# Kernel optimization log

Hardware: AMD Instinct MI355X
Metric: run time of the kernel (lower is better)

## Reference

```python
import jax, jax.numpy as jnp
import numpy as np

N_HEADS = 8
D_HEAD = 64
SCALE = D_HEAD ** -0.5


def setup_inputs() -> dict:
    key = jax.random.key(0)
    k1, k2, k3 = jax.random.split(key, 3)
    B, H, W, C = 16, 32, 32, 512
    ft = jax.random.normal(k1, (B, H, W, C), dtype=jnp.float32)
    # Dense layers: to_qkv -> n_heads*n_dim_heads*3 = 1536 units, to_out -> n_channels
    w_qkv = jax.random.normal(k2, (C, N_HEADS * D_HEAD * 3), dtype=jnp.float32) * (C ** -0.5)
    b_qkv = jnp.zeros((N_HEADS * D_HEAD * 3,), dtype=jnp.float32)
    w_out = jax.random.normal(k3, (N_HEADS * D_HEAD, C), dtype=jnp.float32) * ((N_HEADS * D_HEAD) ** -0.5)
    b_out = jnp.zeros((C,), dtype=jnp.float32)
    return {"ft": ft, "w_qkv": w_qkv, "b_qkv": b_qkv, "w_out": w_out, "b_out": b_out}


def reference(ft, w_qkv, b_qkv, w_out, b_out):
    B, H, W, C = ft.shape
    N = H * W
    x = ft.reshape(B, N, C)                       # b (h w) c
    qkv = x @ w_qkv + b_qkv                       # b n (heads * 3*d_head)
    qkv = qkv.reshape(B, N, N_HEADS, 3 * D_HEAD)  # 'b x (h d) -> b x h d'
    q, k, v = jnp.split(qkv, 3, axis=-1)          # each: b n heads d_head
    attn = jnp.einsum('bxhd,byhd->bxyh', q, k) * SCALE
    attn = jax.nn.softmax(attn, axis=2)           # softmax over key axis y
    res = jnp.einsum('bxyh,byhd->bxhd', attn, v)  # b x h d
    res = res.reshape(B, N, N_HEADS * D_HEAD)     # 'b x h d -> b x (h d)'
    res = res @ w_out + b_out
    res = res + x                                 # residual with pre-qkv flattened input
    return res.reshape(B, H, W, C)
```

## Files before the change

### kernel.cpp

```cpp
#include <hip/hip_runtime.h>
#include <hip/hip_bf16.h>

using u16 = unsigned short;
using u32 = unsigned int;
typedef __attribute__((ext_vector_type(8))) short short8;
typedef __attribute__((ext_vector_type(4))) float f32x4;

#define MFMA16(A, B, C) __builtin_amdgcn_mfma_f32_16x16x32_bf16((A), (B), (C), 0, 0, 0)

__device__ __forceinline__ u16 f2bf(float f) {
  union { float f; u32 i; } v; v.f = f;
  u32 x = v.i;
  return (u16)((x + 0x7fffu + ((x >> 16) & 1u)) >> 16);
}
__device__ __forceinline__ u32 pkbf(float a, float b) {
  union { __hip_bfloat162 h; u32 u; } v;
  v.h = __float22bfloat162_rn(make_float2(a, b));
  return v.u;
}
__device__ __forceinline__ u32 cvtpk(float a, float b) {
  u32 r;
  asm("v_cvt_pk_bf16_f32 %0, %1, %2" : "=v"(r) : "v"(a), "v"(b));
  return r;
}
__device__ __forceinline__ void gl16(const u16* g, u16* l) {
  __builtin_amdgcn_global_load_lds(
      (const __attribute__((address_space(1))) u32*)g,
      (__attribute__((address_space(3))) u32*)l, 16, 0, 0);
}

__global__ __launch_bounds__(256) void conv_x(const float* __restrict__ X,
                                              u16* __restrict__ Xbf) {
  const int i = (blockIdx.x * 256 + threadIdx.x) * 8;
  float4 a = *(const float4*)(X + i);
  float4 b = *(const float4*)(X + i + 4);
  uint4 o;
  o.x = pkbf(a.x, a.y); o.y = pkbf(a.z, a.w);
  o.z = pkbf(b.x, b.y); o.w = pkbf(b.z, b.w);
  *(uint4*)(Xbf + i) = o;
}

__global__ __launch_bounds__(256) void transpose_w(
    const float* __restrict__ Wq, const float* __restrict__ Wo,
    u16* __restrict__ Wqt, u16* __restrict__ Wot) {
  const int z = blockIdx.z;
  if (z == 1 && blockIdx.x >= 16) return;
  const float* src = z ? Wo : Wq;
  u16* dst = z ? Wot : Wqt;
  const int ncols = z ? 512 : 1536;
  __shared__ float tile[32][33];
  const int t = threadIdx.x;
  const int kt = blockIdx.y * 32, nt = blockIdx.x * 32;
  const int r = t >> 3, c4 = (t & 7) * 4;
  float4 v = *(const float4*)(src + (size_t)(kt + r) * ncols + nt + c4);
  tile[r][c4 + 0] = v.x; tile[r][c4 + 1] = v.y;
  tile[r][c4 + 2] = v.z; tile[r][c4 + 3] = v.w;
  __syncthreads();
  uint2 p = make_uint2(pkbf(tile[c4 + 0][r], tile[c4 + 1][r]),
                       pkbf(tile[c4 + 2][r], tile[c4 + 3][r]));
  *(uint2*)(dst + (size_t)(nt + r) * 512 + kt + c4) = p;
}

__global__ __launch_bounds__(512) void qkv_gemm(
    const u16* __restrict__ Xbf, const u16* __restrict__ Wt,
    const float* __restrict__ Bias,
    u16* __restrict__ Qp, u16* __restrict__ Kp, u16* __restrict__ Vt) {
  __shared__ u16 Xs[3][128][32];
  __shared__ u16 Ws[3][256][32];
  const int t = threadIdx.x;
  const int lid = blockIdx.y * 6 + blockIdx.x;
  const int sid = (lid & 7) * 96 + (lid >> 3);
  const int bm = (sid / 6) * 128, bn = (sid % 6) * 256;
  const int w = t >> 6, lane = t & 63, quad = lane >> 4, l16 = lane & 15;
  const int mtb = (w >> 2) * 64, ntb = (w & 3) * 64;
  const int rr = lane >> 2;
  const int gch = ((lane & 3) ^ ((lane >> 3) & 3)) * 8;
  const int sw = (quad ^ ((l16 >> 1) & 3)) * 8;

  const u16* xg0 = Xbf + (size_t)(bm + w * 16 + rr) * 512 + gch;
  const u16* wg0 = Wt + (size_t)(bn + w * 16 + rr) * 512 + gch;
  const u16* wg1 = wg0 + (size_t)128 * 512;

  f32x4 acc[4][4];
  const f32x4 z4 = {0.f, 0.f, 0.f, 0.f};
  #pragma unroll
  for (int mi = 0; mi < 4; mi++)
    #pragma unroll
    for (int ni = 0; ni < 4; ni++) acc[mi][ni] = z4;

  gl16(xg0, &Xs[0][w * 16][0]);
  gl16(wg0, &Ws[0][w * 16][0]); gl16(wg1, &Ws[0][w * 16][0] + 4096);
  gl16(xg0 + 32, &Xs[1][w * 16][0]);
  gl16(wg0 + 32, &Ws[1][w * 16][0]); gl16(wg1 + 32, &Ws[1][w * 16][0] + 4096);
  asm volatile("s_waitcnt vmcnt(3)" ::: "memory");
  __builtin_amdgcn_s_barrier();

  for (int k = 0; k < 16; ++k) {
    const int cur = k % 3;
    if (k < 14) {
      const int nx2 = (k + 2) % 3;
      const int kn = (k + 2) * 32;
      gl16(xg0 + kn, &Xs[nx2][w * 16][0]);
      gl16(wg0 + kn, &Ws[nx2][w * 16][0]);
      gl16(wg1 + kn, &Ws[nx2][w * 16][0] + 4096);
    }
    short8 af[4], bf4[4];
    #pragma unroll
    for (int mi = 0; mi < 4; mi++)
      af[mi] = *(const short8*)&Xs[cur][mtb + mi * 16 + l16][sw];
    #pragma unroll
    for (int ni = 0; ni < 4; ni++)
      bf4[ni] = *(const short8*)&Ws[cur][ntb + ni * 16 + l16][sw];
    #pragma unroll
    for (int mi = 0; mi < 4; mi++)
      #pragma unroll
      for (int ni = 0; ni < 4; ni++)
        acc[mi][ni] = MFMA16(af[mi], bf4[ni], acc[mi][ni]);
    if (k < 15) {
      if (k < 14) asm volatile("s_waitcnt vmcnt(3) lgkmcnt(0)" ::: "memory");
      else        asm volatile("s_waitcnt vmcnt(0) lgkmcnt(0)" ::: "memory");
      __builtin_amdgcn_s_barrier();
    }
  }

  #pragma unroll
  for (int ni = 0; ni < 4; ni++) {
    const int g = bn + ntb + ni * 16;
    const int h = g / 192, rm = g % 192;
    const int type = rm >> 6, dbase = rm & 63;
    const float bias = Bias[g + l16];
    const float qsc = (type == 0) ? 0.125f * 1.44269504088896340736f : 1.0f;
    #pragma unroll
    for (int mi = 0; mi < 4; mi++) {
      const int row0 = bm + mtb + mi * 16 + quad * 4;
      const int b = row0 >> 10, n0 = row0 & 1023;
      const size_t bh = (size_t)(b * 8 + h) * 65536;
      if (type == 2) {
        uint2 p = make_uint2(pkbf(acc[mi][ni][0] + bias, acc[mi][ni][1] + bias),
                             pkbf(acc[mi][ni][2] + bias, acc[mi][ni][3] + bias));
        *(uint2*)(Vt + bh + (size_t)(dbase + l16) * 1024 + n0) = p;
      } else {
        u16* dst = (type ? Kp : Qp) + bh;
        #pragma unroll
        for (int r = 0; r < 4; r++)
          dst[(size_t)(n0 + r) * 64 + dbase + l16] =
              f2bf((acc[mi][ni][r] + bias) * qsc);
      }
    }
  }
}

__global__ __launch_bounds__(512, 8) void attn_mfma(
    const u16* __restrict__ Qp, const u16* __restrict__ Kp,
    const u16* __restrict__ Vt, u16* __restrict__ ATT) {
  __shared__ u16 Ks[2][64][64];
  __shared__ u16 Vs[2][64][64];
  const int t = threadIdx.x, w = t >> 6, lane = t & 63;
  const int quad = lane >> 4, l16 = lane & 15;
  const int bx = blockIdx.x;
  const int c = bx & 7, g = bx >> 3;
  const int qt = g & 7, u = g >> 3;
  const int bh_id = u * 8 + c;
  const int b = bh_id >> 3, h = bh_id & 7;
  const size_t bh = (size_t)bh_id * 65536;
  const u16* Qb = Qp + bh;
  const u16* Kb = Kp + bh;
  const u16* Vb = Vt + bh;
  const int q0 = qt * 128 + w * 16;

  const u16* kg = Kb + (size_t)(t >> 3) * 64 + ((t & 7) ^ ((t >> 3) & 7)) * 8;
  const u16* vg = Vb + (size_t)(t >> 3) * 1024 + ((t & 7) ^ ((t >> 3) & 7)) * 8;
  u16* ks0 = &Ks[0][0][0] + w * 512;
  u16* ks1 = &Ks[1][0][0] + w * 512;
  u16* vs0 = &Vs[0][0][0] + w * 512;
  u16* vs1 = &Vs[1][0][0] + w * 512;

  const int m7 = l16 & 7;
  const char* ksb = (const char*)&Ks[0][0][0];
  const char* vsb = (const char*)&Vs[0][0][0];
  const int kb0 = l16 * 128 + (quad ^ m7) * 16;
  const int kb1 = kb0 ^ 64;
  int vo[2];
  #pragma unroll
  for (int ks = 0; ks < 2; ks++)
    vo[ks] = l16 * 128 + ((4 * ks + quad) ^ m7) * 16;

  short8 qf[2];
  #pragma unroll
  for (int ks = 0; ks < 2; ks++)
    qf[ks] = *(const short8*)(Qb + (size_t)(q0 + l16) * 64 + ks * 32 + quad * 8);

  const short8 vone = {(short)0x3F80, (short)0x3F80, (short)0x3F80,
                       (short)0x3F80, (short)0x3F80, (short)0x3F80,
                       (short)0x3F80, (short)0x3F80};

  f32x4 Of[4], Ol;
  const f32x4 z4 = {0.f, 0.f, 0.f, 0.f};
  #pragma unroll
  for (int ni = 0; ni < 4; ni++) Of[ni] = z4;
  Ol = z4;

  gl16(kg, ks0);
  gl16(vg, vs0);
  __syncthreads();

  for (int kt = 0; kt < 16; ++kt) {
    const int cur = kt & 1;
    if (kt < 15) {
      gl16(kg + (kt + 1) * 4096, cur ? ks0 : ks1);
      gl16(vg + (kt + 1) * 64,   cur ? vs0 : vs1);
    }
    const int co = cur << 13;

    u32 e[4], o[4];
    #pragma unroll
    for (int nt = 0; nt < 4; nt++) {
      short8 k0f = *(const short8*)(ksb + co + kb0 + nt * 2048);
      short8 k1f = *(const short8*)(ksb + co + kb1 + nt * 2048);
      f32x4 s = z4;
      s = MFMA16(k0f, qf[0], s);
      s = MFMA16(k1f, qf[1], s);
      float p0 = __builtin_amdgcn_exp2f(s[0]);
      float p1 = __builtin_amdgcn_exp2f(s[1]);
      float p2 = __builtin_amdgcn_exp2f(s[2]);
      float p3 = __builtin_amdgcn_exp2f(s[3]);
      const u32 lo = cvtpk(p0, p1), hi = cvtpk(p2, p3);
      if (nt & 1) { o[(nt >> 1) * 2] = lo; o[(nt >> 1) * 2 + 1] = hi; }
      else        { e[(nt >> 1) * 2] = lo; e[(nt >> 1) * 2 + 1] = hi; }
    }
    #pragma unroll
    for (int i = 0; i < 4; i++) {
      auto t01 = __builtin_amdgcn_permlane32_swap(e[i], o[i], false, false);
      auto xy  = __builtin_amdgcn_permlane16_swap(t01[0], t01[1], false, false);
      e[i] = xy[0]; o[i] = xy[1];
    }
    #pragma unroll
    for (int ks = 0; ks < 2; ks++) {
      union { short8 v; u32 u[4]; } pa;
      pa.u[0] = e[2 * ks]; pa.u[1] = e[2 * ks + 1];
      pa.u[2] = o[2 * ks]; pa.u[3] = o[2 * ks + 1];
      #pragma unroll
      for (int ni = 0; ni < 4; ni++) {
        short8 vf = *(const short8*)(vsb + co + vo[ks] + ni * 2048);
        Of[ni] = MFMA16(pa.v, vf, Of[ni]);
      }
      Ol = MFMA16(pa.v, vone, Ol);
    }
    __syncthreads();
  }
  #pragma unroll
  for (int r = 0; r < 4; r++) {
    const float inv = 1.0f / Ol[r];
    const int row = b * 1024 + q0 + quad * 4 + r;
    #pragma unroll
    for (int ni = 0; ni < 4; ni++)
      ATT[(size_t)row * 512 + h * 64 + ni * 16 + l16] = f2bf(Of[ni][r] * inv);
  }
}

__global__ __launch_bounds__(512) void out_proj(
    const u16* __restrict__ A, const u16* __restrict__ Wt,
    const float* __restrict__ Bias, const float* __restrict__ FT,
    float* __restrict__ OUT) {
  __shared__ u16 As[3][128][32];
  __shared__ u16 Ws[3][128][32];
  const int t = threadIdx.x;
  const int lid = blockIdx.y * 4 + blockIdx.x;
  const int sid = (lid & 7) * 64 + (lid >> 3);
  const int bm = (sid / 4) * 128, bn = (sid % 4) * 128;
  const int w = t >> 6, lane = t & 63, quad = lane >> 4, l16 = lane & 15;
  const int mtb = (w >> 1) * 32, ntb = (w & 1) * 64;
  const int rr = lane >> 2;
  const int gch = ((lane & 3) ^ ((lane >> 3) & 3)) * 8;
  const int sw = (quad ^ ((l16 >> 1) & 3)) * 8;

  const u16* ag = A + (size_t)(bm + w * 16 + rr) * 512 + gch;
  const u16* wg = Wt + (size_t)(bn + w * 16 + rr) * 512 + gch;

  f32x4 acc[2][4];
  const f32x4 z4 = {0.f, 0.f, 0.f, 0.f};
  #pragma unroll
  for (int mi = 0; mi < 2; mi++)
    #pragma unroll
    for (int ni = 0; ni < 4; ni++) acc[mi][ni] = z4;

  gl16(ag, &As[0][w * 16][0]);      gl16(wg, &Ws[0][w * 16][0]);
  gl16(ag + 32, &As[1][w * 16][0]); gl16(wg + 32, &Ws[1][w * 16][0]);
  asm volatile("s_waitcnt vmcnt(2)" ::: "memory");
  __builtin_amdgcn_s_barrier();

  for (int k = 0; k < 16; ++k) {
    const int cur = k % 3;
    if (k < 14) {
      const int nx2 = (k + 2) % 3;
      const int kn = (k + 2) * 32;
      gl16(ag + kn, &As[nx2][w * 16][0]);
      gl16(wg + kn, &Ws[nx2][w * 16][0]);
    }
    short8 af[2], bf4[4];
    #pragma unroll
    for (int mi = 0; mi < 2; mi++)
      af[mi] = *(const short8*)&As[cur][mtb + mi * 16 + l16][sw];
    #pragma unroll
    for (int ni = 0; ni < 4; ni++)
      bf4[ni] = *(const short8*)&Ws[cur][ntb + ni * 16 + l16][sw];
    #pragma unroll
    for (int mi = 0; mi < 2; mi++)
      #pragma unroll
      for (int ni = 0; ni < 4; ni++)
        acc[mi][ni] = MFMA16(af[mi], bf4[ni], acc[mi][ni]);
    if (k < 15) {
      if (k < 14) asm volatile("s_waitcnt vmcnt(2) lgkmcnt(0)" ::: "memory");
      else        asm volatile("s_waitcnt vmcnt(0) lgkmcnt(0)" ::: "memory");
      __builtin_amdgcn_s_barrier();
    }
  }

  #pragma unroll
  for (int ni = 0; ni < 4; ni++) {
    const int g = bn + ntb + ni * 16;
    const float bias = Bias[g + l16];
    #pragma unroll
    for (int mi = 0; mi < 2; mi++) {
      const int row0 = bm + mtb + mi * 16 + quad * 4;
      #pragma unroll
      for (int r = 0; r < 4; r++) {
        const size_t idx = (size_t)(row0 + r) * 512 + g + l16;
        OUT[idx] = acc[mi][ni][r] + bias + FT[idx];
      }
    }
  }
}

extern "C" void kernel_launch(void* const* d_in, const int* in_sizes, int n_in,
                              void* d_out, int out_size, void* d_ws, size_t ws_size,
                              hipStream_t stream) {
  const float* ft    = (const float*)d_in[0];
  const float* w_qkv = (const float*)d_in[1];
  const float* b_qkv = (const float*)d_in[2];
  const float* w_out = (const float*)d_in[3];
  const float* b_out = (const float*)d_in[4];
  float* out = (float*)d_out;

  char* p = (char*)d_ws;
  u16* Xbf    = (u16*)(p);
  u16* ATT    = Xbf;
  u16* Wqkv_t = (u16*)(p + 16777216);
  u16* Wout_t = (u16*)(p + 18350080);
  u16* Qp     = (u16*)(p + 18874368);
  u16* Kp     = (u16*)(p + 35651584);
  u16* Vt     = (u16*)(p + 52428800);

  conv_x     <<<4096, 256, 0, stream>>>(ft, Xbf);
  transpose_w<<<dim3(48, 16, 2), 256, 0, stream>>>(w_qkv, w_out, Wqkv_t, Wout_t);
  qkv_gemm   <<<dim3(6, 128), 512, 0, stream>>>(Xbf, Wqkv_t, b_qkv, Qp, Kp, Vt);
  attn_mfma  <<<dim3(1024), 512, 0, stream>>>(Qp, Kp, Vt, ATT);
  out_proj   <<<dim3(4, 128), 512, 0, stream>>>(ATT, Wout_t, b_out, ft, out);
}
```

Before: 189.6 us.

## Process two query tiles per wave in attention to reuse K/V fragments

Each wave now handles 32 query rows (two 16-row MFMA tiles) instead of 16, so each K and V fragment read from LDS feeds two MFMAs. The grid is halved to 512 blocks, each covering 256 queries, and the launch-bounds occupancy hint drops from 8 to 4. This cuts LDS reads and global K/V tile loads per query, at the cost of more registers per thread, fewer blocks, and possibly lower occupancy and less latency hiding.

Measured after the change: 182.9 us. -3.5%, faster.

```diff
diff --git a/kernel.cpp b/kernel.cpp
--- a/kernel.cpp
+++ b/kernel.cpp
@@ -150,7 +150,7 @@
   }
 }
 
-__global__ __launch_bounds__(512, 8) void attn_mfma(
+__global__ __launch_bounds__(512, 4) void attn_mfma(
     const u16* __restrict__ Qp, const u16* __restrict__ Kp,
     const u16* __restrict__ Vt, u16* __restrict__ ATT) {
   __shared__ u16 Ks[2][64][64];
@@ -159,14 +159,14 @@
   const int quad = lane >> 4, l16 = lane & 15;
   const int bx = blockIdx.x;
   const int c = bx & 7, g = bx >> 3;
-  const int qt = g & 7, u = g >> 3;
+  const int qt = g & 3, u = g >> 2;
   const int bh_id = u * 8 + c;
   const int b = bh_id >> 3, h = bh_id & 7;
   const size_t bh = (size_t)bh_id * 65536;
   const u16* Qb = Qp + bh;
   const u16* Kb = Kp + bh;
   const u16* Vb = Vt + bh;
-  const int q0 = qt * 128 + w * 16;
+  const int q0 = qt * 256 + w * 32;
 
   const u16* kg = Kb + (size_t)(t >> 3) * 64 + ((t & 7) ^ ((t >> 3) & 7)) * 8;
   const u16* vg = Vb + (size_t)(t >> 3) * 1024 + ((t & 7) ^ ((t >> 3) & 7)) * 8;
@@ -185,20 +185,22 @@
   for (int ks = 0; ks < 2; ks++)
     vo[ks] = l16 * 128 + ((4 * ks + quad) ^ m7) * 16;
 
-  short8 qf[2];
-  #pragma unroll
-  for (int ks = 0; ks < 2; ks++)
-    qf[ks] = *(const short8*)(Qb + (size_t)(q0 + l16) * 64 + ks * 32 + quad * 8);
+  short8 qfA[2], qfB[2];
+  #pragma unroll
+  for (int ks = 0; ks < 2; ks++) {
+    qfA[ks] = *(const short8*)(Qb + (size_t)(q0 + l16) * 64 + ks * 32 + quad * 8);
+    qfB[ks] = *(const short8*)(Qb + (size_t)(q0 + 16 + l16) * 64 + ks * 32 + quad * 8);
+  }
 
   const short8 vone = {(short)0x3F80, (short)0x3F80, (short)0x3F80,
                        (short)0x3F80, (short)0x3F80, (short)0x3F80,
                        (short)0x3F80, (short)0x3F80};
 
-  f32x4 Of[4], Ol;
+  f32x4 OfA[4], OfB[4], OlA, OlB;
   const f32x4 z4 = {0.f, 0.f, 0.f, 0.f};
   #pragma unroll
-  for (int ni = 0; ni < 4; ni++) Of[ni] = z4;
-  Ol = z4;
+  for (int ni = 0; ni < 4; ni++) { OfA[ni] = z4; OfB[ni] = z4; }
+  OlA = z4; OlB = z4;
 
   gl16(kg, ks0);
   gl16(vg, vs0);
@@ -212,49 +214,72 @@
     }
     const int co = cur << 13;
 
-    u32 e[4], o[4];
+    u32 eA[4], oA[4], eB[4], oB[4];
     #pragma unroll
     for (int nt = 0; nt < 4; nt++) {
       short8 k0f = *(const short8*)(ksb + co + kb0 + nt * 2048);
       short8 k1f = *(const short8*)(ksb + co + kb1 + nt * 2048);
-      f32x4 s = z4;
-      s = MFMA16(k0f, qf[0], s);
-      s = MFMA16(k1f, qf[1], s);
-      float p0 = __builtin_amdgcn_exp2f(s[0]);
-      float p1 = __builtin_amdgcn_exp2f(s[1]);
-      float p2 = __builtin_amdgcn_exp2f(s[2]);
-      float p3 = __builtin_amdgcn_exp2f(s[3]);
-      const u32 lo = cvtpk(p0, p1), hi = cvtpk(p2, p3);
-      if (nt & 1) { o[(nt >> 1) * 2] = lo; o[(nt >> 1) * 2 + 1] = hi; }
-      else        { e[(nt >> 1) * 2] = lo; e[(nt >> 1) * 2 + 1] = hi; }
+      f32x4 sA = z4, sB = z4;
+      sA = MFMA16(k0f, qfA[0], sA);
+      sB = MFMA16(k0f, qfB[0], sB);
+      sA = MFMA16(k1f, qfA[1], sA);
+      sB = MFMA16(k1f, qfB[1], sB);
+      float a0 = __builtin_amdgcn_exp2f(sA[0]);
+      float a1 = __builtin_amdgcn_exp2f(sA[1]);
+      float a2 = __builtin_amdgcn_exp2f(sA[2]);
+      float a3 = __builtin_amdgcn_exp2f(sA[3]);
+      float b0 = __builtin_amdgcn_exp2f(sB[0]);
+      float b1 = __builtin_amdgcn_exp2f(sB[1]);
+      float b2 = __builtin_amdgcn_exp2f(sB[2]);
+      float b3 = __builtin_amdgcn_exp2f(sB[3]);
+      const u32 loA = cvtpk(a0, a1), hiA = cvtpk(a2, a3);
+      const u32 loB = cvtpk(b0, b1), hiB = cvtpk(b2, b3);
+      if (nt & 1) {
+        oA[(nt >> 1) * 2] = loA; oA[(nt >> 1) * 2 + 1] = hiA;
+        oB[(nt >> 1) * 2] = loB; oB[(nt >> 1) * 2 + 1] = hiB;
+      } else {
+        eA[(nt >> 1) * 2] = loA; eA[(nt >> 1) * 2 + 1] = hiA;
+        eB[(nt >> 1) * 2] = loB; eB[(nt >> 1) * 2 + 1] = hiB;
+      }
     }
     #pragma unroll
     for (int i = 0; i < 4; i++) {
-      auto t01 = __builtin_amdgcn_permlane32_swap(e[i], o[i], false, false);
-      auto xy  = __builtin_amdgcn_permlane16_swap(t01[0], t01[1], false, false);
-      e[i] = xy[0]; o[i] = xy[1];
+      auto tA = __builtin_amdgcn_permlane32_swap(eA[i], oA[i], false, false);
+      auto xA = __builtin_amdgcn_permlane16_swap(tA[0], tA[1], false, false);
+      eA[i] = xA[0]; oA[i] = xA[1];
+      auto tB = __builtin_amdgcn_permlane32_swap(eB[i], oB[i], false, false);
+      auto xB = __builtin_amdgcn_permlane16_swap(tB[0], tB[1], false, false);
+      eB[i] = xB[0]; oB[i] = xB[1];
     }
     #pragma unroll
     for (int ks = 0; ks < 2; ks++) {
-      union { short8 v; u32 u[4]; } pa;
-      pa.u[0] = e[2 * ks]; pa.u[1] = e[2 * ks + 1];
-      pa.u[2] = o[2 * ks]; pa.u[3] = o[2 * ks + 1];
+      union { short8 v; u32 u[4]; } paA, paB;
+      paA.u[0] = eA[2 * ks]; paA.u[1] = eA[2 * ks + 1];
+      paA.u[2] = oA[2 * ks]; paA.u[3] = oA[2 * ks + 1];
+      paB.u[0] = eB[2 * ks]; paB.u[1] = eB[2 * ks + 1];
+      paB.u[2] = oB[2 * ks]; paB.u[3] = oB[2 * ks + 1];
       #pragma unroll
       for (int ni = 0; ni < 4; ni++) {
         short8 vf = *(const short8*)(vsb + co + vo[ks] + ni * 2048);
-        Of[ni] = MFMA16(pa.v, vf, Of[ni]);
+        OfA[ni] = MFMA16(paA.v, vf, OfA[ni]);
+        OfB[ni] = MFMA16(paB.v, vf, OfB[ni]);
       }
-      Ol = MFMA16(pa.v, vone, Ol);
+      OlA = MFMA16(paA.v, vone, OlA);
+      OlB = MFMA16(paB.v, vone, OlB);
     }
     __syncthreads();
   }
   #pragma unroll
   for (int r = 0; r < 4; r++) {
-    const float inv = 1.0f / Ol[r];
-    const int row = b * 1024 + q0 + quad * 4 + r;
-    #pragma unroll
-    for (int ni = 0; ni < 4; ni++)
-      ATT[(size_t)row * 512 + h * 64 + ni * 16 + l16] = f2bf(Of[ni][r] * inv);
+    const float invA = 1.0f / OlA[r];
+    const float invB = 1.0f / OlB[r];
+    const int rowA = b * 1024 + q0 + quad * 4 + r;
+    const int rowB = rowA + 16;
+    #pragma unroll
+    for (int ni = 0; ni < 4; ni++) {
+      ATT[(size_t)rowA * 512 + h * 64 + ni * 16 + l16] = f2bf(OfA[ni][r] * invA);
+      ATT[(size_t)rowB * 512 + h * 64 + ni * 16 + l16] = f2bf(OfB[ni][r] * invB);
+    }
   }
 }
 
@@ -354,6 +379,6 @@
   conv_x     <<<4096, 256, 0, stream>>>(ft, Xbf);
   transpose_w<<<dim3(48, 16, 2), 256, 0, stream>>>(w_qkv, w_out, Wqkv_t, Wout_t);
   qkv_gemm   <<<dim3(6, 128), 512, 0, stream>>>(Xbf, Wqkv_t, b_qkv, Qp, Kp, Vt);
-  attn_mfma  <<<dim3(1024), 512, 0, stream>>>(Qp, Kp, Vt, ATT);
+  attn_mfma  <<<dim3(512), 512, 0, stream>>>(Qp, Kp, Vt, ATT);
   out_proj   <<<dim3(4, 128), 512, 0, stream>>>(ATT, Wout_t, b_out, ft, out);
 }
```
